# Optimization experiments

Hardware: AMD Instinct MI355X
Metric: run time of the kernel (lower is better)

The kernel has to match this reference:

```python
import jax, jax.numpy as jnp
import numpy as np

N = 10000      # nodes
E = 160000     # edges (before self-loops)
H = 8          # heads
D_IN, D_H1, D_H2 = 165, 128, 1    # per-head channels of gat1 / gat2
HID = H * D_H1                    # 1024


def batchnorm(x, gamma, beta, eps=1e-5):
    # training-mode BatchNorm1d: biased batch statistics over the node axis
    mu = x.mean(0)
    var = x.var(0)
    return (x - mu) * jax.lax.rsqrt(var + eps) * gamma + beta


def gatv2(x, src, dst, Wl, bl, Wr, br, att, bias, heads, out_ch, concat, n_nodes):
    # PyG GATv2Conv: lin_l on source, lin_r on target; e = att . LeakyReLU(xl_j + xr_i)
    xl = (x @ Wl + bl).reshape(n_nodes, heads, out_ch)   # source transform
    xr = (x @ Wr + br).reshape(n_nodes, heads, out_ch)   # target transform
    e = jax.nn.leaky_relu(xl[src] + xr[dst], 0.2)        # [E,H,C]
    logits = jnp.einsum('ehc,hc->eh', e, att)            # [E,H]
    # segment softmax over incoming edges of each destination node
    m = jax.lax.stop_gradient(jax.ops.segment_max(logits, dst, num_segments=n_nodes))
    a = jnp.exp(logits - m[dst])
    s = jax.ops.segment_sum(a, dst, num_segments=n_nodes)
    alpha = a / (s[dst] + 1e-16)                          # [E,H]
    out = jax.ops.segment_sum(xl[src] * alpha[..., None], dst, num_segments=n_nodes)
    out = out.reshape(n_nodes, heads * out_ch) if concat else out.mean(1)
    return out + bias


def setup_inputs() -> dict:
    key = jax.random.key(0)
    ks = jax.random.split(key, 12)
    g = lambda k, shape, fan_in: jax.random.normal(k, shape, jnp.float32) * (1.0 / np.sqrt(fan_in))
    return {
        'x': jax.random.normal(ks[0], (N, D_IN), jnp.float32),
        'gamma1': jnp.ones((D_IN,), jnp.float32),
        'beta1': jnp.zeros((D_IN,), jnp.float32),
        'Wl1': g(ks[1], (D_IN, HID), D_IN),
        'bl1': jnp.zeros((HID,), jnp.float32),
        'Wr1': g(ks[2], (D_IN, HID), D_IN),
        'br1': jnp.zeros((HID,), jnp.float32),
        'att1': g(ks[3], (H, D_H1), D_H1),
        'bias1': jnp.zeros((HID,), jnp.float32),
        'gamma2': jnp.ones((HID,), jnp.float32),
        'beta2': jnp.zeros((HID,), jnp.float32),
        'Wl2': g(ks[4], (HID, H * D_H2), HID),
        'bl2': jnp.zeros((H * D_H2,), jnp.float32),
        'Wr2': g(ks[5], (HID, H * D_H2), HID),
        'br2': jnp.zeros((H * D_H2,), jnp.float32),
        'att2': g(ks[6], (H, D_H2), D_H2),
        'bias2': jnp.zeros((D_H2,), jnp.float32),
        'edge_index': jax.random.randint(ks[7], (2, E), 0, N, jnp.int64 if jax.config.jax_enable_x64 else jnp.int32),
    }


def reference(x, gamma1, beta1, Wl1, bl1, Wr1, br1, att1, bias1,
              gamma2, beta2, Wl2, bl2, Wr2, br2, att2, bias2, edge_index):
    loops = jnp.arange(N, dtype=edge_index.dtype)
    src = jnp.concatenate([edge_index[0], loops])   # add_self_loops=True (PyG default)
    dst = jnp.concatenate([edge_index[1], loops])
    h = batchnorm(x, gamma1, beta1)
    h = gatv2(h, src, dst, Wl1, bl1, Wr1, br1, att1, bias1, H, D_H1, True, N)
    h = batchnorm(h, gamma2, beta2)
    h = jax.nn.leaky_relu(h, 0.01)                  # F.leaky_relu default slope
    out = gatv2(h, src, dst, Wl2, bl2, Wr2, br2, att2, bias2, H, D_H2, False, N)
    return out
```

## Files before the change

kernel.cpp:

```cpp
#include <hip/hip_runtime.h>

#define NN   10000
#define E0   160000
#define ET   170000
#define DIN  165
#define KP   192
#define HID  1024
#define NH   8
#define MAXD 192
#define BP   200
#define K2P  1032


typedef __bf16 bf16x8 __attribute__((ext_vector_type(8)));
typedef float  f32x4  __attribute__((ext_vector_type(4)));

__device__ __forceinline__ float bf2f(unsigned short u) {
    unsigned int i = ((unsigned int)u) << 16;
    return __builtin_bit_cast(float, i);
}
__device__ __forceinline__ unsigned short f2bf(float f) {
    unsigned int i = __builtin_bit_cast(unsigned int, f);
    i += 0x7fffu + ((i >> 16) & 1u);
    return (unsigned short)(i >> 16);
}
__device__ __forceinline__ float fin(float x) {
    return fminf(fmaxf(x, -1e30f), 1e30f);
}
__device__ __forceinline__ int clampi(int s) {
    return min(max(s, 0), NN - 1);
}
__device__ __forceinline__ void unpack8(uint4 u, float* f) {
    f[0]=bf2f((unsigned short)(u.x)); f[1]=bf2f((unsigned short)(u.x>>16));
    f[2]=bf2f((unsigned short)(u.y)); f[3]=bf2f((unsigned short)(u.y>>16));
    f[4]=bf2f((unsigned short)(u.z)); f[5]=bf2f((unsigned short)(u.z>>16));
    f[6]=bf2f((unsigned short)(u.w)); f[7]=bf2f((unsigned short)(u.w>>16));
}

__global__ __launch_bounds__(256) void debug_fill(float* __restrict__ out, float val) {
    int i = blockIdx.x * 256 + threadIdx.x;
    if (i < NN) out[i] = val;
}

__global__ __launch_bounds__(256) void bn1_stats(const float* __restrict__ x,
                                                 float* __restrict__ colsum, float* __restrict__ colsq) {
    int r0 = blockIdx.x * 125;
    int c = threadIdx.x;
    if (c >= DIN) return;
    float acc = 0.f, sq = 0.f;
    for (int r = r0; r < r0 + 125; ++r) {
        float v = x[(size_t)r * DIN + c];
        acc += v; sq += v * v;
    }
    atomicAdd(&colsum[c], acc);
    atomicAdd(&colsq[c], sq);
}

__global__ void bn1_scale(const float* __restrict__ colsum, const float* __restrict__ colsq,
                          const float* __restrict__ gamma, const float* __restrict__ beta,
                          float* __restrict__ A, float* __restrict__ B) {
    int c = threadIdx.x;
    if (c >= DIN) return;
    float mu  = colsum[c] * (1.f / NN);
    float var = fmaxf(colsq[c] * (1.f / NN) - mu * mu, 0.f);
    float a = gamma[c] * rsqrtf(var + 1e-5f);
    A[c] = a; B[c] = beta[c] - mu * a;
}

__global__ __launch_bounds__(256) void bn1_apply(const float* __restrict__ x,
                                                 const float* __restrict__ A, const float* __restrict__ B,
                                                 unsigned short* __restrict__ hn) {
    int idx = blockIdx.x * 256 + threadIdx.x;
    if (idx >= NN * KP) return;
    int r = idx / KP, c = idx - r * KP;
    float v = 0.f;
    if (c < DIN) v = fin(x[(size_t)r * DIN + c] * A[c] + B[c]);
    hn[idx] = f2bf(v);
}

__global__ __launch_bounds__(256) void w1_transpose(const float* __restrict__ wl,
                                                    const float* __restrict__ wr,
                                                    unsigned short* __restrict__ wlt,
                                                    unsigned short* __restrict__ wrt) {
    int idx = blockIdx.x * 256 + threadIdx.x;
    if (idx >= HID * KP) return;
    int n = idx / KP, k = idx - n * KP;
    wlt[idx] = (k < DIN) ? f2bf(wl[(size_t)k * HID + n]) : (unsigned short)0;
    wrt[idx] = (k < DIN) ? f2bf(wr[(size_t)k * HID + n]) : (unsigned short)0;
}

__global__ __launch_bounds__(256) void gemm1_kernel(
    const unsigned short* __restrict__ hn,
    const unsigned short* __restrict__ wlt,
    const unsigned short* __restrict__ wrt,
    const float* __restrict__ bl,
    const float* __restrict__ br,
    unsigned short* __restrict__ xl,
    unsigned short* __restrict__ xr) {
    const unsigned short* wt = blockIdx.z ? wrt : wlt;
    const float* bias        = blockIdx.z ? br  : bl;
    unsigned short* xout     = blockIdx.z ? xr  : xl;

    __shared__ unsigned short bs[64 * BP];
    const int tid  = threadIdx.x;
    const int lane = tid & 63;
    const int wave = tid >> 6;
    const int col  = lane & 15;
    const int q    = lane >> 4;
    const int n0   = blockIdx.y * 64;

    for (int idx = tid; idx < 64 * 48; idx += 256) {
        int r = idx / 48, c = idx - r * 48;
        uint2 v = *(const uint2*)(wt + (size_t)(n0 + r) * KP + c * 4);
        *(uint2*)&bs[r * BP + c * 4] = v;
    }
    __syncthreads();

    const int mbase = blockIdx.x * 128 + wave * 32;
    const int am0 = mbase + col;
    const int am1 = am0 + 16;
    const bool aok0 = (am0 < NN), aok1 = (am1 < NN);

    f32x4 acc[2][4];
    #pragma unroll
    for (int m = 0; m < 2; ++m)
        for (int nt = 0; nt < 4; ++nt)
            for (int r = 0; r < 4; ++r) acc[m][nt][r] = 0.f;

    #pragma unroll
    for (int kt = 0; kt < 6; ++kt) {
        const int kk = kt * 32 + q * 8;
        uint4 a0u = make_uint4(0u,0u,0u,0u), a1u = make_uint4(0u,0u,0u,0u);
        if (aok0) a0u = *(const uint4*)(hn + (size_t)am0 * KP + kk);
        if (aok1) a1u = *(const uint4*)(hn + (size_t)am1 * KP + kk);
        bf16x8 a0 = __builtin_bit_cast(bf16x8, a0u);
        bf16x8 a1 = __builtin_bit_cast(bf16x8, a1u);
        #pragma unroll
        for (int nt = 0; nt < 4; ++nt) {
            bf16x8 bf = __builtin_bit_cast(bf16x8, *(const uint4*)&bs[(nt * 16 + col) * BP + kk]);
            acc[0][nt] = __builtin_amdgcn_mfma_f32_16x16x32_bf16(a0, bf, acc[0][nt], 0, 0, 0);
            acc[1][nt] = __builtin_amdgcn_mfma_f32_16x16x32_bf16(a1, bf, acc[1][nt], 0, 0, 0);
        }
    }

    #pragma unroll
    for (int nt = 0; nt < 4; ++nt) {
        const int nc = n0 + nt * 16 + col;
        const float bv = bias[nc];
        #pragma unroll
        for (int m = 0; m < 2; ++m) {
            #pragma unroll
            for (int r = 0; r < 4; ++r) {
                const int row = mbase + m * 16 + q * 4 + r;
                if (row < NN)
                    xout[(size_t)row * HID + nc] = f2bf(fin(acc[m][nt][r] + bv));
            }
        }
    }
}

__global__ __launch_bounds__(256) void edge_hist(const int* __restrict__ ei, int* __restrict__ deg) {
    int e = blockIdx.x * 256 + threadIdx.x;
    if (e >= ET) return;
    int d = (e < E0) ? ei[E0 + e] : (e - E0);
    atomicAdd(&deg[clampi(d)], 1);
}

__global__ __launch_bounds__(1024) void scan_kernel(const int* __restrict__ deg,
                                                    int* __restrict__ offs, int* __restrict__ cur) {
    __shared__ int wsum[16];
    const int tid = threadIdx.x;
    const int base = tid * 10;
    int loc[10];
    int run = 0;
    #pragma unroll
    for (int j = 0; j < 10; ++j) {
        int idx = base + j;
        int v = (idx < NN) ? deg[idx] : 0;
        loc[j] = run;
        run += v;
    }
    const int lane = tid & 63;
    const int w = tid >> 6;
    int inc = run;
    #pragma unroll
    for (int s = 1; s < 64; s <<= 1) {
        int t = __shfl_up(inc, s);
        if (lane >= s) inc += t;
    }
    if (lane == 63) wsum[w] = inc;
    __syncthreads();
    int woff = 0;
    #pragma unroll
    for (int k = 0; k < 16; ++k) woff += (k < w) ? wsum[k] : 0;
    const int toff = woff + inc - run;
    #pragma unroll
    for (int j = 0; j < 10; ++j) {
        int idx = base + j;
        if (idx < NN) { int e = toff + loc[j]; offs[idx] = e; cur[idx] = e; }
    }
    if (tid == 1023) offs[NN] = woff + inc;
}

__global__ __launch_bounds__(256) void edge_scatter(const int* __restrict__ ei,
                                                    int* __restrict__ cur, int* __restrict__ ssrc) {
    int e = blockIdx.x * 256 + threadIdx.x;
    if (e >= ET) return;
    int s, d;
    if (e < E0) { s = ei[e]; d = ei[E0 + e]; }
    else        { s = e - E0; d = e - E0; }
    int pos = atomicAdd(&cur[clampi(d)], 1);
    if (pos >= 0 && pos < ET) ssrc[pos] = clampi(s);
}

__global__ __launch_bounds__(256) void gat1_node(
    const unsigned short* __restrict__ xl1, const unsigned short* xr1,
    const float* __restrict__ att1, const float* __restrict__ bias1,
    const int* __restrict__ offs, const int* __restrict__ ssrc,
    unsigned short* agg) {
    const int i    = blockIdx.x;
    const int tid  = threadIdx.x;
    const int lane = tid & 63;
    const int wave = tid >> 6;
    __shared__ float o_lds[4][64][16];
    __shared__ float s_lds[4][NH];
    __shared__ int   src_lds[MAXD];
    const int e0 = offs[i];
    const int deg = max(min(offs[i + 1] - e0, MAXD), 0);

    float xr_r[16], att_r[16];
    {
        const uint4* xp = (const uint4*)(xr1 + (size_t)i * HID + lane * 16);
        uint4 u0 = xp[0], u1 = xp[1];
        unpack8(u0, xr_r); unpack8(u1, xr_r + 8);
        const float4* ap = (const float4*)(att1 + lane * 16);
        float4 a0 = ap[0], a1 = ap[1], a2 = ap[2], a3 = ap[3];
        att_r[0]=a0.x; att_r[1]=a0.y; att_r[2]=a0.z; att_r[3]=a0.w;
        att_r[4]=a1.x; att_r[5]=a1.y; att_r[6]=a1.z; att_r[7]=a1.w;
        att_r[8]=a2.x; att_r[9]=a2.y; att_r[10]=a2.z; att_r[11]=a2.w;
        att_r[12]=a3.x; att_r[13]=a3.y; att_r[14]=a3.z; att_r[15]=a3.w;
    }
    for (int e = tid; e < deg; e += 256) src_lds[e] = clampi(ssrc[e0 + e]);
    __syncthreads();

    float o[16];
    #pragma unroll
    for (int j = 0; j < 16; ++j) o[j] = 0.f;
    float s = 0.f;

    for (int e = wave; e < deg; e += 4) {
        const int sidx = src_lds[e];
        const uint4* xp = (const uint4*)(xl1 + (size_t)sidx * HID + lane * 16);
        uint4 u0 = xp[0], u1 = xp[1];
        float xv[16];
        unpack8(u0, xv); unpack8(u1, xv + 8);
        float p = 0.f;
        #pragma unroll
        for (int j = 0; j < 16; ++j) {
            float v = xv[j] + xr_r[j];
            v = fmaxf(v, 0.2f * v);
            p = fmaf(att_r[j], v, p);
        }
        p += __shfl_xor(p, 1); p += __shfl_xor(p, 2); p += __shfl_xor(p, 4);
        const float a = __expf(fminf(fin(p), 50.f));
        s += a;
        #pragma unroll
        for (int j = 0; j < 16; ++j) o[j] = fmaf(a, xv[j], o[j]);
    }

    #pragma unroll
    for (int j = 0; j < 4; ++j)
        *(float4*)&o_lds[wave][lane][j * 4] = make_float4(o[j*4], o[j*4+1], o[j*4+2], o[j*4+3]);
    if ((lane & 7) == 0) s_lds[wave][lane >> 3] = s;
    __syncthreads();

    const int h  = tid >> 5;
    const int lo = tid >> 2;
    const int eo = (tid & 3) * 4;
    const float stot = s_lds[0][h] + s_lds[1][h] + s_lds[2][h] + s_lds[3][h];
    const float inv = 1.f / (stot + 1e-16f);
    float4 r = make_float4(0.f, 0.f, 0.f, 0.f);
    #pragma unroll
    for (int w = 0; w < 4; ++w) {
        float4 t = *(const float4*)&o_lds[w][lo][eo];
        r.x += t.x; r.y += t.y; r.z += t.z; r.w += t.w;
    }
    const float* bp = bias1 + tid * 4;
    ushort4 ov;
    ov.x = f2bf(fin(r.x * inv + bp[0]));
    ov.y = f2bf(fin(r.y * inv + bp[1]));
    ov.z = f2bf(fin(r.z * inv + bp[2]));
    ov.w = f2bf(fin(r.w * inv + bp[3]));
    *(ushort4*)(agg + (size_t)i * HID + tid * 4) = ov;
}

__global__ __launch_bounds__(256) void bn2_stats(const unsigned short* __restrict__ agg,
                                                 float* __restrict__ colsum, float* __restrict__ colsq) {
    int r0 = blockIdx.x * 125;
    int t = threadIdx.x;
    float s0=0,s1=0,s2=0,s3=0,q0=0,q1=0,q2=0,q3=0;
    for (int r = r0; r < r0 + 125; ++r) {
        const ushort4 u = *(const ushort4*)(agg + (size_t)r * HID + t * 4);
        float v0=bf2f(u.x), v1=bf2f(u.y), v2=bf2f(u.z), v3=bf2f(u.w);
        s0+=v0; q0+=v0*v0; s1+=v1; q1+=v1*v1;
        s2+=v2; q2+=v2*v2; s3+=v3; q3+=v3*v3;
    }
    atomicAdd(&colsum[t*4+0], s0); atomicAdd(&colsq[t*4+0], q0);
    atomicAdd(&colsum[t*4+1], s1); atomicAdd(&colsq[t*4+1], q1);
    atomicAdd(&colsum[t*4+2], s2); atomicAdd(&colsq[t*4+2], q2);
    atomicAdd(&colsum[t*4+3], s3); atomicAdd(&colsq[t*4+3], q3);
}

__global__ __launch_bounds__(1024) void bn2_scale(const float* __restrict__ colsum, const float* __restrict__ colsq,
                                                  const float* __restrict__ gamma, const float* __restrict__ beta,
                                                  float* __restrict__ A, float* __restrict__ B) {
    int c = threadIdx.x;
    float mu  = colsum[c] * (1.f / NN);
    float var = fmaxf(colsq[c] * (1.f / NN) - mu * mu, 0.f);
    float a = gamma[c] * rsqrtf(var + 1e-5f);
    A[c] = a; B[c] = beta[c] - mu * a;
}

__global__ __launch_bounds__(256) void bn2_apply(unsigned short* __restrict__ agg,
                                                 const float* __restrict__ A, const float* __restrict__ B) {
    int idx = blockIdx.x * 256 + threadIdx.x;
    int base = idx * 4;
    int c = base & (HID - 1);
    ushort4 u = *(const ushort4*)(agg + base);
    float4 a = *(const float4*)(A + c);
    float4 b = *(const float4*)(B + c);
    float o0 = bf2f(u.x) * a.x + b.x, o1 = bf2f(u.y) * a.y + b.y;
    float o2 = bf2f(u.z) * a.z + b.z, o3 = bf2f(u.w) * a.w + b.w;
    o0 = fmaxf(o0, 0.01f * o0); o1 = fmaxf(o1, 0.01f * o1);
    o2 = fmaxf(o2, 0.01f * o2); o3 = fmaxf(o3, 0.01f * o3);
    ushort4 o; o.x = f2bf(fin(o0)); o.y = f2bf(fin(o1)); o.z = f2bf(fin(o2)); o.w = f2bf(fin(o3));
    *(ushort4*)(agg + base) = o;
}

__global__ __launch_bounds__(256) void w2_prep(const float* __restrict__ wl2,
                                               const float* __restrict__ wr2,
                                               unsigned short* __restrict__ w2ct) {
    int idx = blockIdx.x * 256 + threadIdx.x;
    if (idx >= 16 * HID) return;
    int n = idx >> 10, k = idx & (HID - 1);
    float v = (n < 8) ? wl2[k * 8 + n] : wr2[k * 8 + (n - 8)];
    w2ct[idx] = f2bf(v);
}

__global__ __launch_bounds__(256) void gemm2_kernel(
    const unsigned short* __restrict__ h2,
    const unsigned short* __restrict__ w2ct,
    const float* __restrict__ bl2, const float* __restrict__ br2,
    float* __restrict__ xl2, float* __restrict__ xr2) {
    __shared__ unsigned short bs[16 * K2P];
    const int tid  = threadIdx.x;
    const int lane = tid & 63;
    const int wave = tid >> 6;
    const int col  = lane & 15;
    const int q    = lane >> 4;

    for (int idx = tid; idx < 16 * 256; idx += 256) {
        int r = idx >> 8, c = idx & 255;
        uint2 v = *(const uint2*)(w2ct + (size_t)r * HID + c * 4);
        *(uint2*)&bs[r * K2P + c * 4] = v;
    }
    __syncthreads();

    const int mtile = blockIdx.x * 4 + wave;
    if (mtile >= NN / 16) return;
    const int m0 = mtile * 16;
    const int am = m0 + col;

    f32x4 acc;
    acc[0] = acc[1] = acc[2] = acc[3] = 0.f;
    #pragma unroll
    for (int kt = 0; kt < 32; ++kt) {
        const int kk = kt * 32 + q * 8;
        bf16x8 af = __builtin_bit_cast(bf16x8, *(const uint4*)(h2 + (size_t)am * HID + kk));
        bf16x8 bf = __builtin_bit_cast(bf16x8, *(const uint4*)&bs[col * K2P + kk]);
        acc = __builtin_amdgcn_mfma_f32_16x16x32_bf16(af, bf, acc, 0, 0, 0);
    }

    const float bv = (col < 8) ? bl2[col] : br2[col - 8];
    float* outp = (col < 8) ? (xl2 + col) : (xr2 + (col - 8));
    #pragma unroll
    for (int r = 0; r < 4; ++r) {
        const int row = m0 + q * 4 + r;
        outp[row * 8] = fin(acc[r] + bv);
    }
}

__global__ __launch_bounds__(256) void gat2_node(
    const float* __restrict__ xl2, const float* __restrict__ xr2,
    const float* __restrict__ att2, const float* __restrict__ bias2,
    const int* __restrict__ offs, const int* __restrict__ ssrc,
    float* __restrict__ out) {
    const int lane = threadIdx.x & 63;
    const int wave = threadIdx.x >> 6;
    const int i = blockIdx.x * 4 + wave;
    const int h = lane & 7, slot = lane >> 3;
    const int e0 = offs[i];
    const int e1 = max(offs[i + 1], e0);
    const float xr_h = xr2[i * 8 + h];
    const float att_h = att2[h];
    float m = -1e30f;
    for (int eb = e0; eb < e1; eb += 8) {
        int e = eb + slot;
        float lg = -1e30f;
        if (e < e1) {
            float v = xl2[clampi(ssrc[e]) * 8 + h] + xr_h;
            v = fmaxf(v, 0.2f * v);
            lg = fin(att_h * v);
        }
        m = fmaxf(m, lg);
    }
    m = fmaxf(m, __shfl_xor(m, 8)); m = fmaxf(m, __shfl_xor(m, 16)); m = fmaxf(m, __shfl_xor(m, 32));
    float ssum = 0.f, wsum = 0.f;
    for (int eb = e0; eb < e1; eb += 8) {
        int e = eb + slot;
        if (e < e1) {
            float xlv = xl2[clampi(ssrc[e]) * 8 + h];
            float v = xlv + xr_h;
            v = fmaxf(v, 0.2f * v);
            float a = __expf(fminf(fin(att_h * v) - m, 0.f));
            ssum += a; wsum += a * xlv;
        }
    }
    ssum += __shfl_xor(ssum, 8); ssum += __shfl_xor(ssum, 16); ssum += __shfl_xor(ssum, 32);
    wsum += __shfl_xor(wsum, 8); wsum += __shfl_xor(wsum, 16); wsum += __shfl_xor(wsum, 32);
    float v = fin(wsum / (ssum + 1e-16f));
    v += __shfl_xor(v, 1); v += __shfl_xor(v, 2); v += __shfl_xor(v, 4);
    if (lane == 0) out[i] = fin(v * 0.125f + bias2[0]);
}

extern "C" void kernel_launch(void* const* d_in, const int* in_sizes, int n_in,
                              void* d_out, int out_size, void* d_ws, size_t ws_size,
                              hipStream_t stream) {
    float* out = (float*)d_out;

    static const int expected[18] = {
        NN * DIN, DIN, DIN, DIN * HID, HID, DIN * HID, HID, HID, HID,
        HID, HID, HID * NH, NH, HID * NH, NH, NH, 1, 2 * E0
    };
    if (n_in != 18) {
        debug_fill<<<(NN + 255) / 256, 256, 0, stream>>>(out, 8192.f + 64.f * (float)n_in);
        return;
    }
    for (int i = 0; i < 18; ++i) {
        if (in_sizes[i] != expected[i]) {
            debug_fill<<<(NN + 255) / 256, 256, 0, stream>>>(out, 4096.f + 32.f * (float)i);
            return;
        }
    }

    const float* x      = (const float*)d_in[0];
    const float* gamma1 = (const float*)d_in[1];
    const float* beta1  = (const float*)d_in[2];
    const float* Wl1    = (const float*)d_in[3];
    const float* bl1    = (const float*)d_in[4];
    const float* Wr1    = (const float*)d_in[5];
    const float* br1    = (const float*)d_in[6];
    const float* att1   = (const float*)d_in[7];
    const float* bias1  = (const float*)d_in[8];
    const float* gamma2 = (const float*)d_in[9];
    const float* beta2  = (const float*)d_in[10];
    const float* Wl2    = (const float*)d_in[11];
    const float* bl2    = (const float*)d_in[12];
    const float* Wr2    = (const float*)d_in[13];
    const float* br2    = (const float*)d_in[14];
    const float* att2   = (const float*)d_in[15];
    const float* bias2  = (const float*)d_in[16];
    const int*   ei     = (const int*)d_in[17];

    char* p = (char*)d_ws;
    auto alloc = [&](size_t bytes) -> void* {
        void* r = (void*)p;
        p += (bytes + 255) & ~(size_t)255;
        return r;
    };
    unsigned short* xl1  = (unsigned short*)alloc((size_t)NN * HID * 2);
    unsigned short* xr1  = (unsigned short*)alloc((size_t)NN * HID * 2);
    unsigned short* agg  = xr1;
    unsigned short* hn   = (unsigned short*)alloc((size_t)NN * KP * 2);
    unsigned short* wlt  = (unsigned short*)alloc((size_t)HID * KP * 2);
    unsigned short* wrt  = (unsigned short*)alloc((size_t)HID * KP * 2);
    unsigned short* w2ct = (unsigned short*)alloc((size_t)16 * HID * 2);
    float*          xl2  = (float*)alloc((size_t)NN * 8 * 4);
    float*          xr2  = (float*)alloc((size_t)NN * 8 * 4);
    float*          A1   = (float*)alloc(DIN * 4);
    float*          B1   = (float*)alloc(DIN * 4);
    float*          A2   = (float*)alloc(HID * 4);
    float*          B2   = (float*)alloc(HID * 4);
    int*            offs = (int*)alloc((NN + 1) * 4);
    int*            cur  = (int*)alloc(NN * 4);
    int*            ssrc = (int*)alloc(ET * 4);
    char* zbase = p;
    float* colsum1 = (float*)alloc(DIN * 4);
    float* colsq1  = (float*)alloc(DIN * 4);
    float* colsum2 = (float*)alloc(HID * 4);
    float* colsq2  = (float*)alloc(HID * 4);
    int*   deg     = (int*)alloc(NN * 4);
    size_t zlen = (size_t)(p - zbase);
    hipMemsetAsync(zbase, 0, zlen, stream);

    bn1_stats<<<80, 256, 0, stream>>>(x, colsum1, colsq1);
    bn1_scale<<<1, 256, 0, stream>>>(colsum1, colsq1, gamma1, beta1, A1, B1);
    bn1_apply<<<(NN * KP + 255) / 256, 256, 0, stream>>>(x, A1, B1, hn);
    w1_transpose<<<(HID * KP + 255) / 256, 256, 0, stream>>>(Wl1, Wr1, wlt, wrt);
    gemm1_kernel<<<dim3((NN + 127) / 128, HID / 64, 2), 256, 0, stream>>>(hn, wlt, wrt, bl1, br1, xl1, xr1);
    edge_hist<<<(ET + 255) / 256, 256, 0, stream>>>(ei, deg);
    scan_kernel<<<1, 1024, 0, stream>>>(deg, offs, cur);
    edge_scatter<<<(ET + 255) / 256, 256, 0, stream>>>(ei, cur, ssrc);
    gat1_node<<<NN, 256, 0, stream>>>(xl1, xr1, att1, bias1, offs, ssrc, agg);
    bn2_stats<<<80, 256, 0, stream>>>(agg, colsum2, colsq2);
    bn2_scale<<<1, 1024, 0, stream>>>(colsum2, colsq2, gamma2, beta2, A2, B2);
    bn2_apply<<<(NN * HID / 4 + 255) / 256, 256, 0, stream>>>(agg, A2, B2);
    w2_prep<<<(16 * HID + 255) / 256, 256, 0, stream>>>(Wl2, Wr2, w2ct);
    gemm2_kernel<<<(NN / 16 + 3) / 4, 256, 0, stream>>>(agg, w2ct, bl2, br2, xl2, xr2);
    gat2_node<<<NN / 4, 256, 0, stream>>>(xl2, xr2, att2, bias2, offs, ssrc, out);
}
```

Before: 284.4 us.

## Assign one wavefront per destination node in GAT1 aggregation, unroll edges by two

Measured after the change: 286.7 us. No clear change (+0.8%).

```diff
diff --git a/kernel.cpp b/kernel.cpp
--- a/kernel.cpp
+++ b/kernel.cpp
@@ -7,7 +7,6 @@
 #define KP   192
 #define HID  1024
 #define NH   8
-#define MAXD 192
 #define BP   200
 #define K2P  1032
 
@@ -218,15 +217,11 @@
     const float* __restrict__ att1, const float* __restrict__ bias1,
     const int* __restrict__ offs, const int* __restrict__ ssrc,
     unsigned short* agg) {
-    const int i    = blockIdx.x;
-    const int tid  = threadIdx.x;
-    const int lane = tid & 63;
-    const int wave = tid >> 6;
-    __shared__ float o_lds[4][64][16];
-    __shared__ float s_lds[4][NH];
-    __shared__ int   src_lds[MAXD];
+    const int lane = threadIdx.x & 63;
+    const int wave = threadIdx.x >> 6;
+    const int i = blockIdx.x * 4 + wave;
     const int e0 = offs[i];
-    const int deg = max(min(offs[i + 1] - e0, MAXD), 0);
+    const int e1 = max(offs[i + 1], e0);
 
     float xr_r[16], att_r[16];
     {
@@ -240,16 +235,42 @@
         att_r[8]=a2.x; att_r[9]=a2.y; att_r[10]=a2.z; att_r[11]=a2.w;
         att_r[12]=a3.x; att_r[13]=a3.y; att_r[14]=a3.z; att_r[15]=a3.w;
     }
-    for (int e = tid; e < deg; e += 256) src_lds[e] = clampi(ssrc[e0 + e]);
-    __syncthreads();
 
     float o[16];
     #pragma unroll
     for (int j = 0; j < 16; ++j) o[j] = 0.f;
     float s = 0.f;
 
-    for (int e = wave; e < deg; e += 4) {
-        const int sidx = src_lds[e];
+    int e = e0;
+    for (; e + 1 < e1; e += 2) {
+        const int s0i = clampi(ssrc[e]);
+        const int s1i = clampi(ssrc[e + 1]);
+        const uint4* xp0 = (const uint4*)(xl1 + (size_t)s0i * HID + lane * 16);
+        const uint4* xp1 = (const uint4*)(xl1 + (size_t)s1i * HID + lane * 16);
+        uint4 a0 = xp0[0], a1 = xp0[1], b0 = xp1[0], b1 = xp1[1];
+        float xv0[16], xv1[16];
+        unpack8(a0, xv0); unpack8(a1, xv0 + 8);
+        unpack8(b0, xv1); unpack8(b1, xv1 + 8);
+        float p0 = 0.f, p1 = 0.f;
+        #pragma unroll
+        for (int j = 0; j < 16; ++j) {
+            float v0 = xv0[j] + xr_r[j];
+            float v1 = xv1[j] + xr_r[j];
+            v0 = fmaxf(v0, 0.2f * v0);
+            v1 = fmaxf(v1, 0.2f * v1);
+            p0 = fmaf(att_r[j], v0, p0);
+            p1 = fmaf(att_r[j], v1, p1);
+        }
+        p0 += __shfl_xor(p0, 1); p0 += __shfl_xor(p0, 2); p0 += __shfl_xor(p0, 4);
+        p1 += __shfl_xor(p1, 1); p1 += __shfl_xor(p1, 2); p1 += __shfl_xor(p1, 4);
+        const float aa0 = __expf(fminf(fin(p0), 50.f));
+        const float aa1 = __expf(fminf(fin(p1), 50.f));
+        s += aa0 + aa1;
+        #pragma unroll
+        for (int j = 0; j < 16; ++j) o[j] = fmaf(aa0, xv0[j], fmaf(aa1, xv1[j], o[j]));
+    }
+    if (e < e1) {
+        const int sidx = clampi(ssrc[e]);
         const uint4* xp = (const uint4*)(xl1 + (size_t)sidx * HID + lane * 16);
         uint4 u0 = xp[0], u1 = xp[1];
         float xv[16];
@@ -268,30 +289,17 @@
         for (int j = 0; j < 16; ++j) o[j] = fmaf(a, xv[j], o[j]);
     }
 
-    #pragma unroll
-    for (int j = 0; j < 4; ++j)
-        *(float4*)&o_lds[wave][lane][j * 4] = make_float4(o[j*4], o[j*4+1], o[j*4+2], o[j*4+3]);
-    if ((lane & 7) == 0) s_lds[wave][lane >> 3] = s;
-    __syncthreads();
-
-    const int h  = tid >> 5;
-    const int lo = tid >> 2;
-    const int eo = (tid & 3) * 4;
-    const float stot = s_lds[0][h] + s_lds[1][h] + s_lds[2][h] + s_lds[3][h];
-    const float inv = 1.f / (stot + 1e-16f);
-    float4 r = make_float4(0.f, 0.f, 0.f, 0.f);
-    #pragma unroll
-    for (int w = 0; w < 4; ++w) {
-        float4 t = *(const float4*)&o_lds[w][lo][eo];
-        r.x += t.x; r.y += t.y; r.z += t.z; r.w += t.w;
-    }
-    const float* bp = bias1 + tid * 4;
-    ushort4 ov;
-    ov.x = f2bf(fin(r.x * inv + bp[0]));
-    ov.y = f2bf(fin(r.y * inv + bp[1]));
-    ov.z = f2bf(fin(r.z * inv + bp[2]));
-    ov.w = f2bf(fin(r.w * inv + bp[3]));
-    *(ushort4*)(agg + (size_t)i * HID + tid * 4) = ov;
+    const float inv = 1.f / (s + 1e-16f);
+    const float4* bp = (const float4*)(bias1 + lane * 16);
+    float4 b0 = bp[0], b1 = bp[1], b2 = bp[2], b3 = bp[3];
+    float bb[16] = {b0.x,b0.y,b0.z,b0.w, b1.x,b1.y,b1.z,b1.w,
+                    b2.x,b2.y,b2.z,b2.w, b3.x,b3.y,b3.z,b3.w};
+    unsigned short ov[16];
+    #pragma unroll
+    for (int j = 0; j < 16; ++j) ov[j] = f2bf(fin(o[j] * inv + bb[j]));
+    uint4* op = (uint4*)(agg + (size_t)i * HID + lane * 16);
+    op[0] = *(const uint4*)&ov[0];
+    op[1] = *(const uint4*)&ov[8];
 }
 
 __global__ __launch_bounds__(256) void bn2_stats(const unsigned short* __restrict__ agg,
@@ -511,7 +519,7 @@
     edge_hist<<<(ET + 255) / 256, 256, 0, stream>>>(ei, deg);
     scan_kernel<<<1, 1024, 0, stream>>>(deg, offs, cur);
     edge_scatter<<<(ET + 255) / 256, 256, 0, stream>>>(ei, cur, ssrc);
-    gat1_node<<<NN, 256, 0, stream>>>(xl1, xr1, att1, bias1, offs, ssrc, agg);
+    gat1_node<<<NN / 4, 256, 0, stream>>>(xl1, xr1, att1, bias1, offs, ssrc, agg);
     bn2_stats<<<80, 256, 0, stream>>>(agg, colsum2, colsq2);
     bn2_scale<<<1, 1024, 0, stream>>>(colsum2, colsq2, gamma2, beta2, A2, B2);
     bn2_apply<<<(NN * HID / 4 + 255) / 256, 256, 0, stream>>>(agg, A2, B2);
```
